# Performance work log

Measured on AMD Instinct MI355X. Metric: run time of the kernel, lower is better.

## Reference

```python
import jax, jax.numpy as jnp
import numpy as np

EMBED = 32
HIDDEN = 128
BATCH = 512
SEQ = 512


def setup_inputs() -> dict:
    key = jax.random.key(0)
    k_x, k_wx, k_wh = jax.random.split(key, 3)
    stdu = 1.0 / np.sqrt(HIDDEN)
    x = jax.random.normal(k_x, (BATCH, SEQ, EMBED), dtype=jnp.float32)
    W_x = jax.random.uniform(k_wx, (EMBED, HIDDEN), minval=-stdu, maxval=stdu, dtype=jnp.float32)
    W_h = jax.random.uniform(k_wh, (HIDDEN, HIDDEN), minval=-stdu, maxval=stdu, dtype=jnp.float32)
    b_h = jnp.zeros((HIDDEN,), dtype=jnp.float32)
    return {"x": x, "W_x": W_x, "W_h": W_h, "b_h": b_h}


def reference(x, W_x, W_h, b_h):
    # Elman RNN: h_t = tanh(x_t @ W_x + h_{t-1} @ W_h + b_h)
    B = x.shape[0]
    h0 = jnp.zeros((B, HIDDEN), dtype=x.dtype)
    # Precompute the input projection for all timesteps (same math as per-step matmul)
    xW = jnp.einsum('bte,eh->bth', x, W_x)  # [B, T, H]

    def step(h, xw_t):
        h = jnp.tanh(xw_t + h @ W_h + b_h)
        return h, h

    h_final, out_seq = jax.lax.scan(step, h0, xW.transpose(1, 0, 2))  # out_seq: [T, B, H]
    out = out_seq.transpose(1, 0, 2)  # [B, T, H] (batch_first, like pad_packed output)
    return out, h_final
```

## Files before the change

kernel.cpp:

```cpp
#include <hip/hip_runtime.h>

#define T_SEQ 512
#define EMB 32
#define HID 128
#define BB 2
#define LDSW 160
#define TCH 128

typedef __attribute__((ext_vector_type(8))) short short8;
typedef __attribute__((ext_vector_type(4))) short short4v;
typedef __attribute__((ext_vector_type(4))) float f32x4;

__device__ __forceinline__ short f2bf(float f) {
  union { float f; unsigned u; } v; v.f = f;
  unsigned r = (v.u + 0x7FFFu + ((v.u >> 16) & 1u)) >> 16;
  return (short)r;
}

__device__ __forceinline__ float tanh_fast(float a) {
  float e = __expf(2.0f * a);
  return 1.0f - 2.0f * __builtin_amdgcn_rcpf(e + 1.0f);
}

#define MFMA(a, b, c) __builtin_amdgcn_mfma_f32_16x16x32_bf16((a), (b), (c), 0, 0, 0)

__global__ __launch_bounds__(256) void rnn_fused_kernel(
    const float* __restrict__ x, const float* __restrict__ Wx,
    const float* __restrict__ Wh, const float* __restrict__ bh,
    float* __restrict__ out) {
  __shared__ short hbuf[2][BB][LDSW];
  __shared__ short xlds[TCH][BB][EMB];

  const int tid = threadIdx.x;
  const int wid = tid >> 6;
  const int lane = tid & 63;
  const int l4 = lane >> 4, lm = lane & 15;
  const int row0 = blockIdx.x * BB;
  const int colbase = wid * 32;

  for (int i = tid; i < 2 * BB * LDSW; i += 256) ((short*)hbuf)[i] = 0;

  short8 whf[2][4]; short8 wxf[2]; float bv[2];
#pragma unroll
  for (int nt = 0; nt < 2; ++nt) {
    const int col = colbase + 16 * nt + lm;
    bv[nt] = bh[col];
#pragma unroll
    for (int kb = 0; kb < 4; ++kb) {
      short8 f;
#pragma unroll
      for (int j = 0; j < 8; ++j)
        f[j] = f2bf(Wh[(size_t)(32 * kb + 8 * l4 + j) * HID + col]);
      whf[nt][kb] = f;
    }
    short8 fx;
#pragma unroll
    for (int j = 0; j < 8; ++j)
      fx[j] = f2bf(Wx[(size_t)(8 * l4 + j) * HID + col]);
    wxf[nt] = fx;
  }

  const int rsel = l4 & 1;
  const int csel = l4 >> 1;
  const int ocol = colbase + 16 * csel + lm;

  const unsigned out_off0 =
      ((unsigned)(row0 + rsel) * T_SEQ) * (HID * 4) + (unsigned)ocol * 4;
  float* outb = out;
  float* hfinp = out + (size_t)512 * T_SEQ * HID + (size_t)(row0 + rsel) * HID + ocol;

  const short* hr0 = &hbuf[0][lm & 1][8 * l4];
  const short* hr1 = &hbuf[1][lm & 1][8 * l4];
  short* hw0 = &hbuf[0][rsel][ocol];
  short* hw1 = &hbuf[1][rsel][ocol];
  const short* xbase = &xlds[0][lm & 1][8 * l4];

  const float* xsrc = x + (size_t)row0 * T_SEQ * EMB;

  const f32x4 z_  = {0.f, 0.f, 0.f, 0.f};
  const f32x4 cb0 = {bv[0], bv[0], bv[0], bv[0]};
  const f32x4 cb1 = {bv[1], bv[1], bv[1], bv[1]};

  float th_last = 0.f;

#define RSTEP(T, PAR) do {                                                       \
    const short* hb_ = (PAR) ? hr0 : hr1;                      \
    short8 ah0 = *(const short8*)(hb_ + 0);                                      \
    short8 ah1 = *(const short8*)(hb_ + 32);                                     \
    short8 ah2 = *(const short8*)(hb_ + 64);                                     \
    short8 ah3 = *(const short8*)(hb_ + 96);                                     \
    short8 xa = *(const short8*)(xbase + ((T) & (TCH - 1)) * (BB * EMB));        \
    f32x4 p0 = MFMA(xa, wxf[0], cb0);                                            \
    f32x4 p1 = MFMA(xa, wxf[1], cb1);                                            \
    f32x4 a0 = MFMA(ah0, whf[0][0], z_);                                         \
    f32x4 a1 = MFMA(ah0, whf[1][0], z_);                                         \
    f32x4 b0 = MFMA(ah2, whf[0][2], z_);                                         \
    f32x4 b1 = MFMA(ah2, whf[1][2], z_);                                         \
    a0 = MFMA(ah1, whf[0][1], a0);                                               \
    a1 = MFMA(ah1, whf[1][1], a1);                                               \
    b0 = MFMA(ah3, whf[0][3], b0);                                               \
    b1 = MFMA(ah3, whf[1][3], b1);                                               \
    float vP0 = rsel ? p0[1] : p0[0];                                            \
    float vA0 = rsel ? a0[1] : a0[0];                                            \
    float vB0 = rsel ? b0[1] : b0[0];                                            \
    float vP1 = rsel ? p1[1] : p1[0];                                            \
    float vA1 = rsel ? a1[1] : a1[0];                                            \
    float vB1 = rsel ? b1[1] : b1[0];                                            \
    float v_ = csel ? ((vP1 + vA1) + vB1) : ((vP0 + vA0) + vB0);                 \
    float th_ = tanh_fast(v_);                                                   \
    *((PAR) ? hw1 : hw0) = f2bf(th_);             \
    asm volatile("global_store_dword %0, %1, %2"                                 \
                 :: "v"(out_off0 + (unsigned)(T) * 512u), "v"(th_), "s"(outb));  \
    th_last = th_;                                                               \
    asm volatile("s_waitcnt lgkmcnt(0)\n\ts_barrier" ::: "memory");              \
  } while (0)

  for (int tb = 0; tb < T_SEQ; tb += TCH) {
#pragma unroll
    for (int k = 0; k < (BB * TCH * EMB / 4) / 256; ++k) {
      const int flat4 = tid + k * 256;
      const int e4 = flat4 & 7;
      const int tt = (flat4 >> 3) & (TCH - 1);
      const int r  = flat4 >> 10;
      const f32x4 v4 = *(const f32x4*)(xsrc + (size_t)r * T_SEQ * EMB +
                                       (size_t)(tb + tt) * EMB + e4 * 4);
      short4v s4;
      s4[0] = f2bf(v4[0]); s4[1] = f2bf(v4[1]);
      s4[2] = f2bf(v4[2]); s4[3] = f2bf(v4[3]);
      *(short4v*)&xlds[tt][r][e4 * 4] = s4;
    }
    __syncthreads();

#pragma unroll 4
    for (int t = tb; t < tb + TCH; t += 2) {
      RSTEP(t + 0, 0);
      RSTEP(t + 1, 1);
    }
  }
#undef RSTEP

  *hfinp = th_last;
}

extern "C" void kernel_launch(void* const* d_in, const int* in_sizes, int n_in,
                              void* d_out, int out_size, void* d_ws, size_t ws_size,
                              hipStream_t stream) {
  const float* x  = (const float*)d_in[0];
  const float* Wx = (const float*)d_in[1];
  const float* Wh = (const float*)d_in[2];
  const float* bh = (const float*)d_in[3];
  float* out = (float*)d_out;
  (void)in_sizes; (void)n_in; (void)out_size; (void)d_ws; (void)ws_size;
  rnn_fused_kernel<<<512 / BB, 256, 0, stream>>>(x, Wx, Wh, bh, out);
}
```

Baseline: 136.7 us.

## Stream x directly from global into registers and prefetch x-projection one step ahead

Removes the LDS staging of x chunks and the block-wide syncs that came with them. Each lane now loads its eight x values straight from global memory four timesteps ahead, using a rotating register queue controlled by explicit vmcnt waits. The x@Wx MFMA for the next step is computed during the current step and used as the accumulator seed of the recurrent MFMA chain, which takes it off the serial critical path. This raises register pressure and relies on hand-counted vmcnt values that also have to account for the interleaved output stores.

```diff
diff --git a/kernel.cpp b/kernel.cpp
--- a/kernel.cpp
+++ b/kernel.cpp
@@ -5,15 +5,18 @@
 #define HID 128
 #define BB 2
 #define LDSW 160
-#define TCH 128
 
 typedef __attribute__((ext_vector_type(8))) short short8;
-typedef __attribute__((ext_vector_type(4))) short short4v;
 typedef __attribute__((ext_vector_type(4))) float f32x4;
 
 __device__ __forceinline__ short f2bf(float f) {
   union { float f; unsigned u; } v; v.f = f;
   unsigned r = (v.u + 0x7FFFu + ((v.u >> 16) & 1u)) >> 16;
+  return (short)r;
+}
+
+__device__ __forceinline__ short f2bfu(unsigned u) {
+  unsigned r = (u + 0x7FFFu + ((u >> 16) & 1u)) >> 16;
   return (short)r;
 }
 
@@ -29,7 +32,6 @@
     const float* __restrict__ Wh, const float* __restrict__ bh,
     float* __restrict__ out) {
   __shared__ short hbuf[2][BB][LDSW];
-  __shared__ short xlds[TCH][BB][EMB];
 
   const int tid = threadIdx.x;
   const int wid = tid >> 6;
@@ -64,8 +66,11 @@
   const int csel = l4 >> 1;
   const int ocol = colbase + 16 * csel + lm;
 
+  const unsigned x_off0 =
+      ((unsigned)(row0 + (lm & 1)) * (T_SEQ * EMB) + (unsigned)(8 * l4)) * 4u;
   const unsigned out_off0 =
       ((unsigned)(row0 + rsel) * T_SEQ) * (HID * 4) + (unsigned)ocol * 4;
+  const float* xb = x;
   float* outb = out;
   float* hfinp = out + (size_t)512 * T_SEQ * HID + (size_t)(row0 + rsel) * HID + ocol;
 
@@ -73,9 +78,6 @@
   const short* hr1 = &hbuf[1][lm & 1][8 * l4];
   short* hw0 = &hbuf[0][rsel][ocol];
   short* hw1 = &hbuf[1][rsel][ocol];
-  const short* xbase = &xlds[0][lm & 1][8 * l4];
-
-  const float* xsrc = x + (size_t)row0 * T_SEQ * EMB;
 
   const f32x4 z_  = {0.f, 0.f, 0.f, 0.f};
   const f32x4 cb0 = {bv[0], bv[0], bv[0], bv[0]};
@@ -83,30 +85,66 @@
 
   float th_last = 0.f;
 
-#define RSTEP(T, PAR) do {                                                       \
+  __syncthreads();
+
+  unsigned q00,q01,q02,q03,q04,q05,q06,q07;
+  unsigned q10,q11,q12,q13,q14,q15,q16,q17;
+  unsigned q20,q21,q22,q23,q24,q25,q26,q27;
+  unsigned q30,q31,q32,q33,q34,q35,q36,q37;
+
+#define XL(D, OFF) \
+  asm volatile("global_load_dword %0, %1, %2" : "=v"(D) : "v"(OFF), "s"(xb))
+#define XL8(A0,A1,A2,A3,A4,A5,A6,A7, TT) do {                                    \
+    const unsigned b_ = x_off0 + (unsigned)(TT) * 128u;                          \
+    XL(A0, b_);       XL(A1, b_ + 4u);  XL(A2, b_ + 8u);  XL(A3, b_ + 12u);      \
+    XL(A4, b_ + 16u); XL(A5, b_ + 20u); XL(A6, b_ + 24u); XL(A7, b_ + 28u);      \
+  } while (0)
+
+  XL8(q00,q01,q02,q03,q04,q05,q06,q07, 0);
+  XL8(q10,q11,q12,q13,q14,q15,q16,q17, 1);
+  XL8(q20,q21,q22,q23,q24,q25,q26,q27, 2);
+  XL8(q30,q31,q32,q33,q34,q35,q36,q37, 3);
+
+  f32x4 pA0, pA1, pB0, pB1;
+  asm volatile("s_waitcnt vmcnt(24)" ::: "memory");
+  __builtin_amdgcn_sched_barrier(0);
+  {
+    short8 xa_;
+    xa_[0]=f2bfu(q00); xa_[1]=f2bfu(q01); xa_[2]=f2bfu(q02); xa_[3]=f2bfu(q03);
+    xa_[4]=f2bfu(q04); xa_[5]=f2bfu(q05); xa_[6]=f2bfu(q06); xa_[7]=f2bfu(q07);
+    pA0 = MFMA(xa_, wxf[0], cb0);
+    pA1 = MFMA(xa_, wxf[1], cb1);
+  }
+
+#define RSTEP(T, WN, PAR, C0,C1,C2,C3,C4,C5,C6,C7, F0,F1,F2,F3,F4,F5,F6,F7,     \
+              PIN0, PIN1, POUT0, POUT1) do {                                     \
     const short* hb_ = (PAR) ? hr0 : hr1;                      \
     short8 ah0 = *(const short8*)(hb_ + 0);                                      \
     short8 ah1 = *(const short8*)(hb_ + 32);                                     \
     short8 ah2 = *(const short8*)(hb_ + 64);                                     \
     short8 ah3 = *(const short8*)(hb_ + 96);                                     \
-    short8 xa = *(const short8*)(xbase + ((T) & (TCH - 1)) * (BB * EMB));        \
-    f32x4 p0 = MFMA(xa, wxf[0], cb0);                                            \
-    f32x4 p1 = MFMA(xa, wxf[1], cb1);                                            \
-    f32x4 a0 = MFMA(ah0, whf[0][0], z_);                                         \
-    f32x4 a1 = MFMA(ah0, whf[1][0], z_);                                         \
+    f32x4 a0 = MFMA(ah0, whf[0][0], PIN0);                 \
+    f32x4 a1 = MFMA(ah0, whf[1][0], PIN1);                                       \
     f32x4 b0 = MFMA(ah2, whf[0][2], z_);                                         \
     f32x4 b1 = MFMA(ah2, whf[1][2], z_);                                         \
     a0 = MFMA(ah1, whf[0][1], a0);                                               \
     a1 = MFMA(ah1, whf[1][1], a1);                                               \
     b0 = MFMA(ah3, whf[0][3], b0);                                               \
     b1 = MFMA(ah3, whf[1][3], b1);                                               \
-    float vP0 = rsel ? p0[1] : p0[0];                                            \
+    asm volatile("s_waitcnt vmcnt(" #WN ")" ::: "memory");                       \
+    __builtin_amdgcn_sched_barrier(0);                                           \
+    short8 xa_;                                                                  \
+    xa_[0]=f2bfu(C0); xa_[1]=f2bfu(C1); xa_[2]=f2bfu(C2); xa_[3]=f2bfu(C3);      \
+    xa_[4]=f2bfu(C4); xa_[5]=f2bfu(C5); xa_[6]=f2bfu(C6); xa_[7]=f2bfu(C7);      \
+    { int tl_ = (T) + 4; if (tl_ > T_SEQ - 1) tl_ = T_SEQ - 1;                   \
+      XL8(F0,F1,F2,F3,F4,F5,F6,F7, tl_); }                                       \
+    POUT0 = MFMA(xa_, wxf[0], cb0);                       \
+    POUT1 = MFMA(xa_, wxf[1], cb1);                                              \
     float vA0 = rsel ? a0[1] : a0[0];                                            \
     float vB0 = rsel ? b0[1] : b0[0];                                            \
-    float vP1 = rsel ? p1[1] : p1[0];                                            \
     float vA1 = rsel ? a1[1] : a1[0];                                            \
     float vB1 = rsel ? b1[1] : b1[0];                                            \
-    float v_ = csel ? ((vP1 + vA1) + vB1) : ((vP0 + vA0) + vB0);                 \
+    float v_ = csel ? (vA1 + vB1) : (vA0 + vB0);                                 \
     float th_ = tanh_fast(v_);                                                   \
     *((PAR) ? hw1 : hw0) = f2bf(th_);             \
     asm volatile("global_store_dword %0, %1, %2"                                 \
@@ -115,29 +153,27 @@
     asm volatile("s_waitcnt lgkmcnt(0)\n\ts_barrier" ::: "memory");              \
   } while (0)
 
-  for (int tb = 0; tb < T_SEQ; tb += TCH) {
-#pragma unroll
-    for (int k = 0; k < (BB * TCH * EMB / 4) / 256; ++k) {
-      const int flat4 = tid + k * 256;
-      const int e4 = flat4 & 7;
-      const int tt = (flat4 >> 3) & (TCH - 1);
-      const int r  = flat4 >> 10;
-      const f32x4 v4 = *(const f32x4*)(xsrc + (size_t)r * T_SEQ * EMB +
-                                       (size_t)(tb + tt) * EMB + e4 * 4);
-      short4v s4;
-      s4[0] = f2bf(v4[0]); s4[1] = f2bf(v4[1]);
-      s4[2] = f2bf(v4[2]); s4[3] = f2bf(v4[3]);
-      *(short4v*)&xlds[tt][r][e4 * 4] = s4;
-    }
-    __syncthreads();
-
-#pragma unroll 4
-    for (int t = tb; t < tb + TCH; t += 2) {
-      RSTEP(t + 0, 0);
-      RSTEP(t + 1, 1);
-    }
+  RSTEP(0, 16, 0, q10,q11,q12,q13,q14,q15,q16,q17,
+                  q00,q01,q02,q03,q04,q05,q06,q07, pA0,pA1, pB0,pB1);
+  RSTEP(1, 17, 1, q20,q21,q22,q23,q24,q25,q26,q27,
+                  q10,q11,q12,q13,q14,q15,q16,q17, pB0,pB1, pA0,pA1);
+  RSTEP(2, 18, 0, q30,q31,q32,q33,q34,q35,q36,q37,
+                  q20,q21,q22,q23,q24,q25,q26,q27, pA0,pA1, pB0,pB1);
+  RSTEP(3, 19, 1, q00,q01,q02,q03,q04,q05,q06,q07,
+                  q30,q31,q32,q33,q34,q35,q36,q37, pB0,pB1, pA0,pA1);
+  for (int tb = 4; tb < T_SEQ; tb += 4) {
+    RSTEP(tb + 0, 19, 0, q10,q11,q12,q13,q14,q15,q16,q17,
+                         q00,q01,q02,q03,q04,q05,q06,q07, pA0,pA1, pB0,pB1);
+    RSTEP(tb + 1, 19, 1, q20,q21,q22,q23,q24,q25,q26,q27,
+                         q10,q11,q12,q13,q14,q15,q16,q17, pB0,pB1, pA0,pA1);
+    RSTEP(tb + 2, 19, 0, q30,q31,q32,q33,q34,q35,q36,q37,
+                         q20,q21,q22,q23,q24,q25,q26,q27, pA0,pA1, pB0,pB1);
+    RSTEP(tb + 3, 19, 1, q00,q01,q02,q03,q04,q05,q06,q07,
+                         q30,q31,q32,q33,q34,q35,q36,q37, pB0,pB1, pA0,pA1);
   }
 #undef RSTEP
+#undef XL8
+#undef XL
 
   *hfinp = th_last;
 }
```

Result: slower. 190.2 us (+39.1%).
